# Kernel tuning notes

Measured on AMD Instinct MI355X. Metric: run time of the kernel, lower is better.

The kernel has to match this reference:

```python
import jax, jax.numpy as jnp
import numpy as np


def setup_inputs() -> dict:
    key = jax.random.key(0)
    ks = jax.random.split(key, 9)
    B, Nq, Nkv, C, ICO = 1, 512, 2562, 64, 64
    return {
        "q": jax.random.normal(ks[0], (B, Nq, C), jnp.float32),
        "q_coord": jax.random.normal(ks[1], (B, Nq, 3), jnp.float32),
        "kv": jax.random.normal(ks[2], (B, Nkv, ICO), jnp.float32),
        "kv_coord": jax.random.normal(ks[3], (B, Nkv, 3), jnp.float32),
        "Wq": jax.random.normal(ks[4], (C, C), jnp.float32) * (C ** -0.5),
        "Wkv": jax.random.normal(ks[5], (ICO, 2 * C), jnp.float32) * (ICO ** -0.5),
        "Wdelta": jax.random.normal(ks[6], (3, C), jnp.float32) * (3 ** -0.5),
        "Wproj": jax.random.normal(ks[7], (C, C), jnp.float32) * (C ** -0.5),
        "bproj": jnp.zeros((C,), jnp.float32),
    }


def reference(q, q_coord, kv, kv_coord, Wq, Wkv, Wdelta, Wproj, bproj):
    C = q.shape[-1]
    scale = 1.0 / C  # erp_dim ** -1 (qk_scale=None)
    q_ = q @ Wq                                   # [B, Nq, C]
    kv_ = kv @ Wkv                                # [B, Nkv, 2C]
    k, v = jnp.split(kv_, 2, axis=-1)             # each [B, Nkv, C]
    # positional encoding: exp(-|dq - dk|) over 3D coords, projected to C
    pos_enc = jnp.exp(-jnp.abs(q_coord[:, :, None] - kv_coord[:, None])) @ Wdelta  # [B,Nq,Nkv,C]
    # elementwise abs-diff attention score, reduced over channel dim
    score = (jnp.exp(-jnp.abs(q_[:, :, None] - k[:, None])) + pos_enc).sum(-1) * scale  # [B,Nq,Nkv]
    attn = jax.nn.softmax(score, axis=-1)
    out = attn @ v                                # [B, Nq, C]
    return out @ Wproj + bproj
```

## Files before the change

kernel.cpp:

```cpp
#include <hip/hip_runtime.h>

#define NQ   512
#define NKV  2562
#define CH   64
#define QB   2
#define BT   1024

#define KVROWS 8
#define NKVB ((NKV + KVROWS - 1) / KVROWS)
#define QROWS 16
#define NQB (NQ / QROWS)

#define E(a, b) __expf(-fabsf((a) - (b)))

__global__ __launch_bounds__(256) void gemm_qkv(
    const float* __restrict__ q, const float* __restrict__ kv,
    const float* __restrict__ Wq, const float* __restrict__ Wkv,
    float* __restrict__ qp, float* __restrict__ kvp) {
  const int tid = threadIdx.x;
  if (blockIdx.x < NKVB) {
    const int j0 = blockIdx.x * KVROWS;
    __shared__ float s_in[KVROWS][CH];
    if (tid < KVROWS * (CH / 4)) {
      int r = tid >> 4, g = tid & 15;
      int j = j0 + r;
      float4 v = (j < NKV) ? ((const float4*)(kv + (size_t)j * CH))[g]
                           : make_float4(0.f, 0.f, 0.f, 0.f);
      ((float4*)&s_in[r][0])[g] = v;
    }
    __syncthreads();
    const int r = tid >> 5;
    const int mg = (tid & 31) * 4;
    float4 acc = make_float4(0.f, 0.f, 0.f, 0.f);
#pragma unroll 16
    for (int rr = 0; rr < CH; ++rr) {
      float a = s_in[r][rr];
      float4 w = *(const float4*)(Wkv + (size_t)rr * 2 * CH + mg);
      acc.x = fmaf(a, w.x, acc.x); acc.y = fmaf(a, w.y, acc.y);
      acc.z = fmaf(a, w.z, acc.z); acc.w = fmaf(a, w.w, acc.w);
    }
    int j = j0 + r;
    if (j < NKV) *(float4*)(kvp + (size_t)j * 2 * CH + mg) = acc;
  } else {
    const int i0 = (blockIdx.x - NKVB) * QROWS;
    __shared__ float s_in[QROWS][CH];
    {
      int r = tid >> 4, g = tid & 15;
      float4 v = ((const float4*)(q + (size_t)(i0 + r) * CH))[g];
      ((float4*)&s_in[r][0])[g] = v;
    }
    __syncthreads();
    const int r = tid >> 4;
    const int cg = (tid & 15) * 4;
    float4 acc = make_float4(0.f, 0.f, 0.f, 0.f);
#pragma unroll 16
    for (int rr = 0; rr < CH; ++rr) {
      float a = s_in[r][rr];
      float4 w = *(const float4*)(Wq + (size_t)rr * CH + cg);
      acc.x = fmaf(a, w.x, acc.x); acc.y = fmaf(a, w.y, acc.y);
      acc.z = fmaf(a, w.z, acc.z); acc.w = fmaf(a, w.w, acc.w);
    }
    *(float4*)(qp + (size_t)(i0 + r) * CH + cg) = acc;
  }
}

__global__ __launch_bounds__(BT, 4) void attn_kernel(
    const float* __restrict__ qp, const float* __restrict__ kvp,
    const float* __restrict__ qc, const float* __restrict__ kvc,
    const float* __restrict__ Wdelta, const float* __restrict__ Wproj,
    const float* __restrict__ bproj, float* __restrict__ out) {
  __shared__ float s_score[QB][NKV];
  __shared__ float s_red[QB][BT];
  __shared__ float s_out[QB][CH];
  __shared__ float s_wd[3];

  const int i0 = blockIdx.x * QB;
  const int tid = threadIdx.x;
  const int sub = tid & 3;
  const int c0 = sub * 16;
  const int wid = tid >> 6;
  const int lane = tid & 63;

  if (tid < 3) {
    float s = 0.f;
    for (int c = 0; c < CH; ++c) s += Wdelta[tid * CH + c];
    s_wd[tid] = s;
  }

  const float4* q0p = (const float4*)(qp + (size_t)i0 * CH + c0);
  const float4* q1p = (const float4*)(qp + (size_t)(i0 + 1) * CH + c0);
  float4 qa0 = q0p[0], qa1 = q0p[1], qa2 = q0p[2], qa3 = q0p[3];
  float4 qb0 = q1p[0], qb1 = q1p[1], qb2 = q1p[2], qb3 = q1p[3];
  asm volatile("" : "+v"(qa0.x), "+v"(qa0.y), "+v"(qa0.z), "+v"(qa0.w),
                    "+v"(qa1.x), "+v"(qa1.y), "+v"(qa1.z), "+v"(qa1.w),
                    "+v"(qa2.x), "+v"(qa2.y), "+v"(qa2.z), "+v"(qa2.w),
                    "+v"(qa3.x), "+v"(qa3.y), "+v"(qa3.z), "+v"(qa3.w));
  asm volatile("" : "+v"(qb0.x), "+v"(qb0.y), "+v"(qb0.z), "+v"(qb0.w),
                    "+v"(qb1.x), "+v"(qb1.y), "+v"(qb1.z), "+v"(qb1.w),
                    "+v"(qb2.x), "+v"(qb2.y), "+v"(qb2.z), "+v"(qb2.w),
                    "+v"(qb3.x), "+v"(qb3.y), "+v"(qb3.z), "+v"(qb3.w));

  float qc0[3], qc1[3];
#pragma unroll
  for (int d = 0; d < 3; ++d) {
    qc0[d] = qc[(size_t)i0 * 3 + d];
    qc1[d] = qc[(size_t)(i0 + 1) * 3 + d];
  }
  __syncthreads();
  const float wd0 = s_wd[0], wd1 = s_wd[1], wd2 = s_wd[2];
  const float scale = 1.0f / 64.0f;

  float lmax0 = -1e30f, lmax1 = -1e30f;
  for (int j = tid >> 2; j < NKV; j += BT / 4) {
    const float4* kr = (const float4*)(kvp + (size_t)j * 2 * CH + c0);
    float4 k0 = kr[0], k1 = kr[1], k2 = kr[2], k3 = kr[3];
    float s0 = ((E(qa0.x, k0.x) + E(qa0.y, k0.y)) + (E(qa0.z, k0.z) + E(qa0.w, k0.w)))
             + ((E(qa1.x, k1.x) + E(qa1.y, k1.y)) + (E(qa1.z, k1.z) + E(qa1.w, k1.w)))
             + ((E(qa2.x, k2.x) + E(qa2.y, k2.y)) + (E(qa2.z, k2.z) + E(qa2.w, k2.w)))
             + ((E(qa3.x, k3.x) + E(qa3.y, k3.y)) + (E(qa3.z, k3.z) + E(qa3.w, k3.w)));
    float s1 = ((E(qb0.x, k0.x) + E(qb0.y, k0.y)) + (E(qb0.z, k0.z) + E(qb0.w, k0.w)))
             + ((E(qb1.x, k1.x) + E(qb1.y, k1.y)) + (E(qb1.z, k1.z) + E(qb1.w, k1.w)))
             + ((E(qb2.x, k2.x) + E(qb2.y, k2.y)) + (E(qb2.z, k2.z) + E(qb2.w, k2.w)))
             + ((E(qb3.x, k3.x) + E(qb3.y, k3.y)) + (E(qb3.z, k3.z) + E(qb3.w, k3.w)));
    s0 += __shfl_xor(s0, 1); s0 += __shfl_xor(s0, 2);
    s1 += __shfl_xor(s1, 1); s1 += __shfl_xor(s1, 2);
    if (sub == 0) {
      float d0 = kvc[(size_t)j * 3 + 0], d1 = kvc[(size_t)j * 3 + 1], d2 = kvc[(size_t)j * 3 + 2];
      s0 += E(qc0[0], d0) * wd0 + E(qc0[1], d1) * wd1 + E(qc0[2], d2) * wd2;
      s1 += E(qc1[0], d0) * wd0 + E(qc1[1], d1) * wd1 + E(qc1[2], d2) * wd2;
      s0 *= scale; s1 *= scale;
      s_score[0][j] = s0; s_score[1][j] = s1;
      lmax0 = fmaxf(lmax0, s0); lmax1 = fmaxf(lmax1, s1);
    }
  }

#pragma unroll
  for (int off = 1; off < 64; off <<= 1) {
    lmax0 = fmaxf(lmax0, __shfl_xor(lmax0, off));
    lmax1 = fmaxf(lmax1, __shfl_xor(lmax1, off));
  }
  if (lane == 0) { s_red[0][wid] = lmax0; s_red[1][wid] = lmax1; }
  __syncthreads();
  float m0 = s_red[0][0], m1 = s_red[1][0];
#pragma unroll
  for (int w = 1; w < BT / 64; ++w) {
    m0 = fmaxf(m0, s_red[0][w]);
    m1 = fmaxf(m1, s_red[1][w]);
  }
  __syncthreads();

  float ls0 = 0.f, ls1 = 0.f;
  for (int j = tid; j < NKV; j += BT) {
    float p0 = __expf(s_score[0][j] - m0); s_score[0][j] = p0; ls0 += p0;
    float p1 = __expf(s_score[1][j] - m1); s_score[1][j] = p1; ls1 += p1;
  }
#pragma unroll
  for (int off = 1; off < 64; off <<= 1) {
    ls0 += __shfl_xor(ls0, off);
    ls1 += __shfl_xor(ls1, off);
  }
  if (lane == 0) { s_red[0][wid] = ls0; s_red[1][wid] = ls1; }
  __syncthreads();
  float t0 = s_red[0][0], t1 = s_red[1][0];
#pragma unroll
  for (int w = 1; w < BT / 64; ++w) { t0 += s_red[0][w]; t1 += s_red[1][w]; }
  const float inv0 = 1.0f / t0, inv1 = 1.0f / t1;
  __syncthreads();

  const int c = tid & 63, g = tid >> 6;
  float a0 = 0.f, a1 = 0.f;
#pragma unroll 4
  for (int j = g; j < NKV; j += 16) {
    float v = kvp[(size_t)j * 128 + 64 + c];
    a0 = fmaf(s_score[0][j], v, a0);
    a1 = fmaf(s_score[1][j], v, a1);
  }
  s_red[0][tid] = a0; s_red[1][tid] = a1;
  __syncthreads();
  if (g == 0) {
    float u0 = 0.f, u1 = 0.f;
#pragma unroll
    for (int gg = 0; gg < 16; ++gg) {
      u0 += s_red[0][gg * 64 + c];
      u1 += s_red[1][gg * 64 + c];
    }
    s_out[0][c] = u0 * inv0;
    s_out[1][c] = u1 * inv1;
  }
  __syncthreads();

  float p0 = 0.f, p1 = 0.f;
#pragma unroll
  for (int r0 = 0; r0 < 4; ++r0) {
    int r = g * 4 + r0;
    float w = Wproj[r * CH + c];
    p0 = fmaf(s_out[0][r], w, p0);
    p1 = fmaf(s_out[1][r], w, p1);
  }
  s_red[0][tid] = p0; s_red[1][tid] = p1;
  __syncthreads();
  if (g == 0) {
    float u0 = 0.f, u1 = 0.f;
#pragma unroll
    for (int gg = 0; gg < 16; ++gg) {
      u0 += s_red[0][gg * 64 + c];
      u1 += s_red[1][gg * 64 + c];
    }
    out[i0 * CH + c] = u0 + bproj[c];
    out[(i0 + 1) * CH + c] = u1 + bproj[c];
  }
}

extern "C" void kernel_launch(void* const* d_in, const int* in_sizes, int n_in,
                              void* d_out, int out_size, void* d_ws, size_t ws_size,
                              hipStream_t stream) {
  const float* q      = (const float*)d_in[0];
  const float* qc     = (const float*)d_in[1];
  const float* kv     = (const float*)d_in[2];
  const float* kvc    = (const float*)d_in[3];
  const float* Wq     = (const float*)d_in[4];
  const float* Wkv    = (const float*)d_in[5];
  const float* Wdelta = (const float*)d_in[6];
  const float* Wproj  = (const float*)d_in[7];
  const float* bproj  = (const float*)d_in[8];
  float* outp = (float*)d_out;

  float* qp  = (float*)d_ws;
  float* kvp = qp + NQ * CH;

  gemm_qkv<<<NKVB + NQB, 256, 0, stream>>>(q, kv, Wq, Wkv, qp, kvp);
  attn_kernel<<<NQ / QB, BT, 0, stream>>>(qp, kvp, qc, kvc, Wdelta, Wproj, bproj, outp);
}
```

Before: 110.8 us.

## Split KV range across two blocks per query pair and merge softmax partials

Measured after the change: 142.8 us. +28.9%, slower.

```diff
diff --git a/kernel.cpp b/kernel.cpp
--- a/kernel.cpp
+++ b/kernel.cpp
@@ -5,6 +5,8 @@
 #define CH   64
 #define QB   2
 #define BT   1024
+#define JH   1281
+#define PSTRIDE 132
 
 #define KVROWS 8
 #define NKVB ((NKV + KVROWS - 1) / KVROWS)
@@ -64,17 +66,19 @@
   }
 }
 
-__global__ __launch_bounds__(BT, 4) void attn_kernel(
+__global__ __launch_bounds__(BT, 8) void attn_part(
     const float* __restrict__ qp, const float* __restrict__ kvp,
     const float* __restrict__ qc, const float* __restrict__ kvc,
-    const float* __restrict__ Wdelta, const float* __restrict__ Wproj,
-    const float* __restrict__ bproj, float* __restrict__ out) {
-  __shared__ float s_score[QB][NKV];
+    const float* __restrict__ Wdelta, float* __restrict__ part) {
+  __shared__ float s_score[QB][JH];
   __shared__ float s_red[QB][BT];
-  __shared__ float s_out[QB][CH];
   __shared__ float s_wd[3];
 
-  const int i0 = blockIdx.x * QB;
+  const int qpair = blockIdx.x >> 1;
+  const int h = blockIdx.x & 1;
+  const int i0 = qpair * QB;
+  const int jlo = h * JH, jhi = jlo + JH;
+
   const int tid = threadIdx.x;
   const int sub = tid & 3;
   const int c0 = sub * 16;
@@ -111,7 +115,7 @@
   const float scale = 1.0f / 64.0f;
 
   float lmax0 = -1e30f, lmax1 = -1e30f;
-  for (int j = tid >> 2; j < NKV; j += BT / 4) {
+  for (int j = jlo + (tid >> 2); j < jhi; j += BT / 4) {
     const float4* kr = (const float4*)(kvp + (size_t)j * 2 * CH + c0);
     float4 k0 = kr[0], k1 = kr[1], k2 = kr[2], k3 = kr[3];
     float s0 = ((E(qa0.x, k0.x) + E(qa0.y, k0.y)) + (E(qa0.z, k0.z) + E(qa0.w, k0.w)))
@@ -129,7 +133,7 @@
       s0 += E(qc0[0], d0) * wd0 + E(qc0[1], d1) * wd1 + E(qc0[2], d2) * wd2;
       s1 += E(qc1[0], d0) * wd0 + E(qc1[1], d1) * wd1 + E(qc1[2], d2) * wd2;
       s0 *= scale; s1 *= scale;
-      s_score[0][j] = s0; s_score[1][j] = s1;
+      s_score[0][j - jlo] = s0; s_score[1][j - jlo] = s1;
       lmax0 = fmaxf(lmax0, s0); lmax1 = fmaxf(lmax1, s1);
     }
   }
@@ -150,9 +154,9 @@
   __syncthreads();
 
   float ls0 = 0.f, ls1 = 0.f;
-  for (int j = tid; j < NKV; j += BT) {
-    float p0 = __expf(s_score[0][j] - m0); s_score[0][j] = p0; ls0 += p0;
-    float p1 = __expf(s_score[1][j] - m1); s_score[1][j] = p1; ls1 += p1;
+  for (int jj = tid; jj < JH; jj += BT) {
+    float p0 = __expf(s_score[0][jj] - m0); s_score[0][jj] = p0; ls0 += p0;
+    float p1 = __expf(s_score[1][jj] - m1); s_score[1][jj] = p1; ls1 += p1;
   }
 #pragma unroll
   for (int off = 1; off < 64; off <<= 1) {
@@ -164,19 +168,20 @@
   float t0 = s_red[0][0], t1 = s_red[1][0];
 #pragma unroll
   for (int w = 1; w < BT / 64; ++w) { t0 += s_red[0][w]; t1 += s_red[1][w]; }
-  const float inv0 = 1.0f / t0, inv1 = 1.0f / t1;
   __syncthreads();
 
   const int c = tid & 63, g = tid >> 6;
   float a0 = 0.f, a1 = 0.f;
 #pragma unroll 4
-  for (int j = g; j < NKV; j += 16) {
+  for (int j = jlo + g; j < jhi; j += 16) {
     float v = kvp[(size_t)j * 128 + 64 + c];
-    a0 = fmaf(s_score[0][j], v, a0);
-    a1 = fmaf(s_score[1][j], v, a1);
+    a0 = fmaf(s_score[0][j - jlo], v, a0);
+    a1 = fmaf(s_score[1][j - jlo], v, a1);
   }
   s_red[0][tid] = a0; s_red[1][tid] = a1;
   __syncthreads();
+
+  float* P = part + (size_t)(qpair * 2 + h) * PSTRIDE;
   if (g == 0) {
     float u0 = 0.f, u1 = 0.f;
 #pragma unroll
@@ -184,31 +189,39 @@
       u0 += s_red[0][gg * 64 + c];
       u1 += s_red[1][gg * 64 + c];
     }
-    s_out[0][c] = u0 * inv0;
-    s_out[1][c] = u1 * inv1;
-  }
-  __syncthreads();
-
-  float p0 = 0.f, p1 = 0.f;
-#pragma unroll
-  for (int r0 = 0; r0 < 4; ++r0) {
-    int r = g * 4 + r0;
-    float w = Wproj[r * CH + c];
-    p0 = fmaf(s_out[0][r], w, p0);
-    p1 = fmaf(s_out[1][r], w, p1);
-  }
-  s_red[0][tid] = p0; s_red[1][tid] = p1;
-  __syncthreads();
-  if (g == 0) {
-    float u0 = 0.f, u1 = 0.f;
-#pragma unroll
-    for (int gg = 0; gg < 16; ++gg) {
-      u0 += s_red[0][gg * 64 + c];
-      u1 += s_red[1][gg * 64 + c];
-    }
-    out[i0 * CH + c] = u0 + bproj[c];
-    out[(i0 + 1) * CH + c] = u1 + bproj[c];
-  }
+    P[4 + c] = u0;
+    P[68 + c] = u1;
+    if (c == 0) { P[0] = m0; P[1] = t0; P[2] = m1; P[3] = t1; }
+  }
+}
+
+__global__ __launch_bounds__(256) void attn_merge(
+    const float* __restrict__ part, const float* __restrict__ Wproj,
+    const float* __restrict__ bproj, float* __restrict__ out) {
+  __shared__ float s_o[4][CH];
+  const int tid = threadIdx.x;
+  const int g = tid >> 6, c = tid & 63;
+  const int i = blockIdx.x * 4 + g;
+  const int qp = i >> 1, qs = i & 1;
+
+  const float* P0 = part + (size_t)(qp * 2 + 0) * PSTRIDE;
+  const float* P1 = part + (size_t)(qp * 2 + 1) * PSTRIDE;
+  const float m_0 = P0[2 * qs], s_0 = P0[2 * qs + 1];
+  const float m_1 = P1[2 * qs], s_1 = P1[2 * qs + 1];
+  const float o_0 = P0[4 + qs * 64 + c];
+  const float o_1 = P1[4 + qs * 64 + c];
+
+  const float m = fmaxf(m_0, m_1);
+  const float w0 = __expf(m_0 - m), w1 = __expf(m_1 - m);
+  const float inv = 1.0f / (w0 * s_0 + w1 * s_1);
+  s_o[g][c] = (w0 * o_0 + w1 * o_1) * inv;
+  __syncthreads();
+
+  float acc = 0.f;
+#pragma unroll 16
+  for (int r = 0; r < CH; ++r)
+    acc = fmaf(s_o[g][r], Wproj[r * CH + c], acc);
+  out[(size_t)i * CH + c] = acc + bproj[c];
 }
 
 extern "C" void kernel_launch(void* const* d_in, const int* in_sizes, int n_in,
@@ -225,9 +238,11 @@
   const float* bproj  = (const float*)d_in[8];
   float* outp = (float*)d_out;
 
-  float* qp  = (float*)d_ws;
-  float* kvp = qp + NQ * CH;
+  float* qp   = (float*)d_ws;
+  float* kvp  = qp + NQ * CH;
+  float* part = kvp + (size_t)NKV * 2 * CH;
 
   gemm_qkv<<<NKVB + NQB, 256, 0, stream>>>(q, kv, Wq, Wkv, qp, kvp);
-  attn_kernel<<<NQ / QB, BT, 0, stream>>>(qp, kvp, qc, kvc, Wdelta, Wproj, bproj, outp);
-}
+  attn_part<<<(NQ / QB) * 2, BT, 0, stream>>>(qp, kvp, qc, kvc, Wdelta, part);
+  attn_merge<<<NQ / 4, 256, 0, stream>>>(part, Wproj, bproj, outp);
+}
```
